# Kernel tuning notes

Measured on AMD Instinct MI355X. Metric: run time of the kernel, lower is better.

## Reference

```python
import jax, jax.numpy as jnp
import numpy as np

P = 3            # spline degree per axis (cubic)
NC = 64          # control points per axis
DOUT = 3         # output dimension of control points
NQ = 1_000_000   # number of query points


def open_uniform_knots(n, p):
    interior = np.linspace(0.0, 1.0, n - p + 1)
    return np.concatenate([np.zeros(p), interior, np.ones(p)]).astype(np.float32)  # len n+p+1


def bspline_basis(t, p, x):
    """Cox-de Boor basis. t:[n+p+1], x:[N] -> (i:[N,p+1] int, b:[N,p+1] float)."""
    n_basis = t.shape[0] - p - 1
    t_clamped = jnp.clip(x, t[p], t[-p - 1])
    k = jnp.searchsorted(t, t_clamped, side='right') - 1
    k = jnp.clip(k, p, n_basis - 1)                       # [N]
    i = k[:, None] + jnp.arange(-p, 1)                    # [N, p+1] global basis idx
    d = jnp.broadcast_to(jnp.eye(p + 1, dtype=x.dtype), (x.shape[0], p + 1, p + 1))
    for r in range(1, p + 1):
        j = jnp.arange(p, r - 1, -1)                      # [p-r+1]
        jk = j[None, :] + k[:, None]                      # [N, p-r+1]
        left = t[jk - p]
        right = t[jk + 1 - r]
        alpha = ((x[:, None] - left) / (right - left))[..., None]  # [N, p-r+1, 1]
        d = d.at[:, j].set((1.0 - alpha) * d[:, j - 1] + alpha * d[:, j])
    return i, d[:, p]                                     # basis values sum to 1


def setup_inputs() -> dict:
    key = jax.random.key(0)
    kq, kc = jax.random.split(key)
    queries = jax.random.uniform(kq, (NQ, 3), dtype=jnp.float32)
    control_points = jax.random.normal(kc, (NC * NC * NC, DOUT), dtype=jnp.float32)
    t = jnp.asarray(open_uniform_knots(NC, P))
    return {"queries": queries, "control_points": control_points,
            "tx": t, "ty": t, "tz": t}


def reference(queries, control_points, tx, ty, tz):
    px = py = pz = P
    ix, bx = bspline_basis(tx, px, queries[:, 0])   # [N,px+1]
    iy, by = bspline_basis(ty, py, queries[:, 1])
    iz, bz = bspline_basis(tz, pz, queries[:, 2])
    nx = tx.shape[0] - px - 1
    ny = ty.shape[0] - py - 1
    # flat index into [nx*ny*nz] control grid: ix + nx*(iy + ny*iz)
    flat_idx = (ix[:, :, None, None]
                + nx * (iy[:, None, :, None] + ny * iz[:, None, None, :]))  # [N,px+1,py+1,pz+1]
    cp_sel = control_points[flat_idx]                   # [N,px+1,py+1,pz+1,DOUT]
    y = jnp.einsum('na,nb,nc,nabcd->nd', bx, by, bz, cp_sel)
    return y
```

## Files before the change

kernel.cpp:

```cpp
#include <hip/hip_runtime.h>


#define NC 64
#define NSEG 61
#define NCELLS 512
#define WDIM 11
#define CAP 2560
#define CHUNK 512
#define NCHUNK 5
#define CHUNK_S 2048
#define OVF_CAP 4096
#define NB 512
#define FCHUNK 1024
#define FNCHUNK 3

typedef float vfloat4 __attribute__((ext_vector_type(4)));

__device__ __forceinline__ float rcpf(float x) {
#if __has_builtin(__builtin_amdgcn_rcpf)
  return __builtin_amdgcn_rcpf(x);
#else
  return 1.0f / x;
#endif
}

__device__ __forceinline__ int span_of(float x) {
  float xc = fminf(fmaxf(x, 0.0f), 1.0f);
  int j = (int)floorf(xc * (float)NSEG);
  return j > NSEG - 1 ? NSEG - 1 : (j < 0 ? 0 : j);
}

__device__ __forceinline__ float knotv(int i) {
  float v = (float)(i - 3) * (1.0f / (float)NSEG);
  return fminf(fmaxf(v, 0.0f), 1.0f);
}

__device__ __forceinline__ void basis4(float x, int j, float N[4]) {
  float xc = fminf(fmaxf(x, 0.0f), 1.0f);
  int k = j + 3;
  float left[4], right[4];
  N[0] = 1.0f;
#pragma unroll
  for (int jj = 1; jj <= 3; ++jj) {
    left[jj] = xc - knotv(k + 1 - jj);
    right[jj] = knotv(k + jj) - xc;
    float saved = 0.0f;
#pragma unroll
    for (int r = 0; r < jj; ++r) {
      float temp = N[r] * rcpf(right[r + 1] + left[jj - r]);
      N[r] = saved + right[r + 1] * temp;
      saved = left[jj - r] * temp;
    }
    N[jj] = saved;
  }
}

__device__ __forceinline__ void eval_point(float x, float y, float z, int jx,
                                           int jy, int jz,
                                           const float* __restrict__ cp,
                                           float o[3]) {
  float Nx[4], Ny[4], Nz[4];
  basis4(x, jx, Nx);
  basis4(y, jy, Ny);
  basis4(z, jz, Nz);
  float ax = 0, ay = 0, az = 0;
#pragma unroll 1
  for (int c = 0; c < 4; ++c) {
#pragma unroll
    for (int b = 0; b < 4; ++b) {
      float w = Ny[b] * Nz[c];
      const float* row = cp + 3 * (size_t)(jx + NC * (jy + b + NC * (jz + c)));
      vfloat4 f0, f1, f2;
      __builtin_memcpy(&f0, row + 0, 16);
      __builtin_memcpy(&f1, row + 4, 16);
      __builtin_memcpy(&f2, row + 8, 16);
      ax += w * (Nx[0] * f0.x + Nx[1] * f0.w + Nx[2] * f1.z + Nx[3] * f2.y);
      ay += w * (Nx[0] * f0.y + Nx[1] * f1.x + Nx[2] * f1.w + Nx[3] * f2.z);
      az += w * (Nx[0] * f0.z + Nx[1] * f1.y + Nx[2] * f2.x + Nx[3] * f2.w);
    }
  }
  o[0] = ax; o[1] = ay; o[2] = az;
}


__global__ __launch_bounds__(256) void scatter_capped(
    const float* __restrict__ q, int* __restrict__ gcursor,
    int* __restrict__ ovfcnt, float4* __restrict__ ovf,
    float4* __restrict__ sorted, int nq) {
  __shared__ int lh[NCELLS];
  __shared__ int lcur[NCELLS];
  int b = blockIdx.x, tid = threadIdx.x;
  for (int c = tid; c < NCELLS; c += 256) { lh[c] = 0; lcur[c] = 0; }
  __syncthreads();

  int s = b * CHUNK_S, e = min(nq, s + CHUNK_S);
  float xs[8], ys[8], zs[8];
  int cells[8];
#pragma unroll
  for (int it = 0; it < 8; ++it) {
    int i = s + it * 256 + tid;
    cells[it] = -1;
    if (i < e) {
      float xyz[3];
      __builtin_memcpy(xyz, q + 3 * (size_t)i, 12);
      xs[it] = xyz[0]; ys[it] = xyz[1]; zs[it] = xyz[2];
      int cell = (span_of(xyz[0]) >> 3) + 8 * (span_of(xyz[1]) >> 3) +
                 64 * (span_of(xyz[2]) >> 3);
      cells[it] = cell;
      atomicAdd(&lh[cell], 1);
    }
  }
  __syncthreads();
  for (int c = tid; c < NCELLS; c += 256) {
    int n = lh[c];
    lh[c] = n ? atomicAdd(&gcursor[c], n) : 0;
  }
  __syncthreads();
#pragma unroll
  for (int it = 0; it < 8; ++it) {
    int cell = cells[it];
    if (cell < 0) continue;
    int i = s + it * 256 + tid;
    int r = lh[cell] + atomicAdd(&lcur[cell], 1);
    if (r < CAP) {
      int jx = span_of(xs[it]), jy = span_of(ys[it]), jz = span_of(zs[it]);
      unsigned u = (unsigned)i | ((unsigned)(jx & 7) << 20) |
                   ((unsigned)(jy & 7) << 23) | ((unsigned)(jz & 7) << 26);
      sorted[(size_t)cell * CAP + r] =
          make_float4(xs[it], ys[it], zs[it], __int_as_float((int)u));
    } else {
      int p = atomicAdd(ovfcnt, 1);
      if (p < OVF_CAP)
        ovf[p] = make_float4(xs[it], ys[it], zs[it], __int_as_float(i));
    }
  }
}

__global__ __launch_bounds__(256) void eval_kernel(
    const float4* __restrict__ sorted, const int* __restrict__ cellbase,
    const int* __restrict__ cellcnt, const float* __restrict__ cp,
    float* __restrict__ out, int use_cap) {
  int cid = blockIdx.x / NCHUNK;
  int chunkid = blockIdx.x % NCHUNK;
  int cnt = cellcnt[cid];
  if (use_cap) cnt = min(cnt, CAP);
  if (chunkid * CHUNK >= cnt) return;
  size_t base = use_cap ? (size_t)cid * CAP : (size_t)cellbase[cid];
  int ox = (cid & 7) * 8, oy = ((cid >> 3) & 7) * 8, oz = (cid >> 6) * 8;

  __shared__ float4 lds[WDIM * WDIM * WDIM];
  for (int e = threadIdx.x; e < WDIM * WDIM * WDIM; e += 256) {
    int lx = e % WDIM, t = e / WDIM;
    int ly = t % WDIM, lz = t / WDIM;
    int gx = min(ox + lx, NC - 1), gy = min(oy + ly, NC - 1),
        gz = min(oz + lz, NC - 1);
    const float* p = cp + 3 * (size_t)(gx + NC * (gy + NC * gz));
    lds[e] = make_float4(p[0], p[1], p[2], 0.0f);
  }
  __syncthreads();

  for (int q0 = chunkid * CHUNK; q0 < cnt; q0 += NCHUNK * CHUNK) {
    int qend = min(cnt, q0 + CHUNK);
    for (int qi = q0 + (int)threadIdx.x; qi < qend; qi += 256) {
      float4 s = sorted[base + qi];
      unsigned u = (unsigned)__float_as_int(s.w);
      int oi = (int)(u & 0xFFFFFu);
      int lx0 = (int)((u >> 20) & 7), ly0 = (int)((u >> 23) & 7),
          lz0 = (int)((u >> 26) & 7);
      float Nx[4], Ny[4], Nz[4];
      basis4(s.x, ox + lx0, Nx);
      basis4(s.y, oy + ly0, Ny);
      basis4(s.z, oz + lz0, Nz);

      float ax = 0.0f, ay = 0.0f, az = 0.0f;
#pragma unroll
      for (int c = 0; c < 4; ++c) {
#pragma unroll
        for (int b = 0; b < 4; ++b) {
          float w = Ny[b] * Nz[c];
          const float4* row = &lds[((lz0 + c) * WDIM + (ly0 + b)) * WDIM + lx0];
          float4 p0 = row[0], p1 = row[1], p2 = row[2], p3 = row[3];
          ax += w * (Nx[0] * p0.x + Nx[1] * p1.x + Nx[2] * p2.x + Nx[3] * p3.x);
          ay += w * (Nx[0] * p0.y + Nx[1] * p1.y + Nx[2] * p2.y + Nx[3] * p3.y);
          az += w * (Nx[0] * p0.z + Nx[1] * p1.z + Nx[2] * p2.z + Nx[3] * p3.z);
        }
      }
      float o[3] = {ax, ay, az};
      __builtin_memcpy(out + 3 * (size_t)oi, o, 12);
    }
  }
}

__global__ __launch_bounds__(256) void ovf_kernel(const float4* __restrict__ ovf,
                                                  const int* __restrict__ ovfcnt,
                                                  const float* __restrict__ cp,
                                                  float* __restrict__ out) {
  int n = min(*ovfcnt, OVF_CAP);
  for (int i = blockIdx.x * 256 + threadIdx.x; i < n; i += gridDim.x * 256) {
    float4 s = ovf[i];
    int oi = __float_as_int(s.w);
    float o[3];
    eval_point(s.x, s.y, s.z, span_of(s.x), span_of(s.y), span_of(s.z), cp, o);
    __builtin_memcpy(out + 3 * (size_t)oi, o, 12);
  }
}


__global__ __launch_bounds__(256) void hist_kernel(const float* __restrict__ q,
                                                   int* __restrict__ histmat,
                                                   int nq, int chunk) {
  __shared__ int lh[NCELLS];
  for (int c = threadIdx.x; c < NCELLS; c += 256) lh[c] = 0;
  __syncthreads();
  int b = blockIdx.x;
  int s = b * chunk, e = min(nq, s + chunk);
  for (int i = s + (int)threadIdx.x; i < e; i += 256) {
    float xyz[3];
    __builtin_memcpy(xyz, q + 3 * (size_t)i, 12);
    int cell = (span_of(xyz[0]) >> 3) + 8 * (span_of(xyz[1]) >> 3) +
               64 * (span_of(xyz[2]) >> 3);
    atomicAdd(&lh[cell], 1);
  }
  __syncthreads();
  for (int c = threadIdx.x; c < NCELLS; c += 256)
    histmat[(size_t)c * NB + b] = lh[c];
}

__global__ __launch_bounds__(512) void rowscan_kernel(int* __restrict__ histmat,
                                                      int* __restrict__ cellsum) {
  __shared__ int sh[NB];
  int c = blockIdx.x, tid = threadIdx.x;
  int v = histmat[(size_t)c * NB + tid];
  sh[tid] = v;
  __syncthreads();
  for (int off = 1; off < NB; off <<= 1) {
    int t = (tid >= off) ? sh[tid - off] : 0;
    __syncthreads();
    sh[tid] += t;
    __syncthreads();
  }
  histmat[(size_t)c * NB + tid] = sh[tid] - v;
  if (tid == NB - 1) cellsum[c] = sh[tid];
}

__global__ __launch_bounds__(512) void cellscan_kernel(const int* __restrict__ cellsum,
                                                       int* __restrict__ cellbase) {
  __shared__ int sh[NCELLS];
  int tid = threadIdx.x;
  int v = cellsum[tid];
  sh[tid] = v;
  __syncthreads();
  for (int off = 1; off < NCELLS; off <<= 1) {
    int t = (tid >= off) ? sh[tid - off] : 0;
    __syncthreads();
    sh[tid] += t;
    __syncthreads();
  }
  cellbase[tid] = sh[tid] - v;
}

__global__ __launch_bounds__(256) void scatter_scan(const float* __restrict__ q,
                                                    const int* __restrict__ histmat,
                                                    const int* __restrict__ cellbase,
                                                    float4* __restrict__ sorted,
                                                    int nq, int chunk) {
  __shared__ int lcur[NCELLS];
  __shared__ int gbase[NCELLS];
  int b = blockIdx.x;
  for (int c = threadIdx.x; c < NCELLS; c += 256) {
    lcur[c] = 0;
    gbase[c] = cellbase[c] + histmat[(size_t)c * NB + b];
  }
  __syncthreads();
  int s = b * chunk, e = min(nq, s + chunk);
  for (int i = s + (int)threadIdx.x; i < e; i += 256) {
    float xyz[3];
    __builtin_memcpy(xyz, q + 3 * (size_t)i, 12);
    int jx = span_of(xyz[0]), jy = span_of(xyz[1]), jz = span_of(xyz[2]);
    int cell = (jx >> 3) + 8 * (jy >> 3) + 64 * (jz >> 3);
    int r = atomicAdd(&lcur[cell], 1);
    unsigned u = (unsigned)i | ((unsigned)(jx & 7) << 20) |
                 ((unsigned)(jy & 7) << 23) | ((unsigned)(jz & 7) << 26);
    sorted[gbase[cell] + r] =
        make_float4(xyz[0], xyz[1], xyz[2], __int_as_float((int)u));
  }
}

__global__ __launch_bounds__(256) void spline_direct_kernel(
    const float* __restrict__ q, const float* __restrict__ cp,
    float* __restrict__ out, int nq) {
  int i = blockIdx.x * 256 + threadIdx.x;
  if (i >= nq) return;
  float xyz[3];
  __builtin_memcpy(xyz, q + 3 * (size_t)i, 12);
  float o[3];
  eval_point(xyz[0], xyz[1], xyz[2], span_of(xyz[0]), span_of(xyz[1]),
             span_of(xyz[2]), cp, o);
  __builtin_memcpy(out + 3 * (size_t)i, o, 12);
}

extern "C" void kernel_launch(void* const* d_in, const int* in_sizes, int n_in,
                              void* d_out, int out_size, void* d_ws,
                              size_t ws_size, hipStream_t stream) {
  const float* queries = (const float*)d_in[0];
  const float* control = (const float*)d_in[1];
  float* out = (float*)d_out;
  int nq = in_sizes[0] / 3;

  size_t meta_c = (NCELLS + 1) * sizeof(int);
  size_t meta_cp = (meta_c + 15) & ~15ull;
  size_t need_c = meta_cp + (size_t)OVF_CAP * 16 + (size_t)NCELLS * CAP * 16;
  size_t meta_s = (size_t)NCELLS * NB * 4 + 2 * NCELLS * 4;
  size_t need_s = ((meta_s + 15) & ~15ull) + (size_t)nq * 16;

  if (nq < (1 << 20) && ws_size >= need_c) {
    int* gcursor = (int*)d_ws;
    int* ovfcnt = gcursor + NCELLS;
    float4* ovf = (float4*)((char*)d_ws + meta_cp);
    float4* sorted = ovf + OVF_CAP;
    hipMemsetAsync(d_ws, 0, meta_c, stream);
    int nb = (nq + CHUNK_S - 1) / CHUNK_S;
    scatter_capped<<<nb, 256, 0, stream>>>(queries, gcursor, ovfcnt, ovf,
                                           sorted, nq);
    eval_kernel<<<NCELLS * NCHUNK, 256, 0, stream>>>(sorted, gcursor, gcursor,
                                                     control, out, 1);
    ovf_kernel<<<4, 256, 0, stream>>>(ovf, ovfcnt, control, out);
  } else if (nq < (1 << 20) && ws_size >= need_s) {
    int* histmat = (int*)d_ws;
    int* cellsum = histmat + (size_t)NCELLS * NB;
    int* cellbase = cellsum + NCELLS;
    float4* sorted = (float4*)((char*)d_ws + ((meta_s + 15) & ~15ull));
    int chunk = (nq + NB - 1) / NB;
    hist_kernel<<<NB, 256, 0, stream>>>(queries, histmat, nq, chunk);
    rowscan_kernel<<<NCELLS, 512, 0, stream>>>(histmat, cellsum);
    cellscan_kernel<<<1, 512, 0, stream>>>(cellsum, cellbase);
    scatter_scan<<<NB, 256, 0, stream>>>(queries, histmat, cellbase, sorted,
                                         nq, chunk);
    eval_kernel<<<NCELLS * FNCHUNK, 256, 0, stream>>>(sorted, cellbase, cellsum,
                                                      control, out, 0);
  } else {
    spline_direct_kernel<<<(nq + 255) / 256, 256, 0, stream>>>(queries, control,
                                                               out, nq);
  }
}
```

Before: 141.8 us.

## Stage scatter writes in LDS by cell and sub-sort eval points by local span

The capped scatter kernel now does a block-local exclusive scan over cell counts and stages points in shared memory in cell order. It then writes them to the global bins in a second pass, so consecutive threads store to consecutive addresses instead of scattering randomly. The eval kernel bins the points of each chunk by their 9-bit local span key and processes them in that order, so a wavefront touches similar LDS control-point windows. The unused histogram/scan fallback path is removed. The added scans and syncs cost extra LDS traffic and barriers, and scatter_capped now uses about 44 KB of LDS, which may lower occupancy.

```diff
diff --git a/kernel.cpp b/kernel.cpp
--- a/kernel.cpp
+++ b/kernel.cpp
@@ -10,9 +10,6 @@
 #define NCHUNK 5
 #define CHUNK_S 2048
 #define OVF_CAP 4096
-#define NB 512
-#define FCHUNK 1024
-#define FNCHUNK 3
 
 typedef float vfloat4 __attribute__((ext_vector_type(4)));
 
@@ -82,20 +79,42 @@
   o[0] = ax; o[1] = ay; o[2] = az;
 }
 
+__device__ __forceinline__ void scan512_excl(int* arr) {
+  int tid = threadIdx.x;
+  int c0 = arr[tid], c1 = arr[tid + 256];
+#pragma unroll
+  for (int off = 1; off < 512; off <<= 1) {
+    int t0 = (tid >= off) ? arr[tid - off] : 0;
+    int t1 = ((tid + 256) >= off) ? arr[tid + 256 - off] : 0;
+    __syncthreads();
+    arr[tid] += t0;
+    arr[tid + 256] += t1;
+    __syncthreads();
+  }
+  arr[tid] -= c0;
+  arr[tid + 256] -= c1;
+  __syncthreads();
+}
+
 
 __global__ __launch_bounds__(256) void scatter_capped(
     const float* __restrict__ q, int* __restrict__ gcursor,
     int* __restrict__ ovfcnt, float4* __restrict__ ovf,
     float4* __restrict__ sorted, int nq) {
-  __shared__ int lh[NCELLS];
+  __shared__ int hist[NCELLS];
+  __shared__ int gb[NCELLS];
   __shared__ int lcur[NCELLS];
+  __shared__ float4 stage[CHUNK_S];
+  __shared__ int addr[CHUNK_S];
   int b = blockIdx.x, tid = threadIdx.x;
-  for (int c = tid; c < NCELLS; c += 256) { lh[c] = 0; lcur[c] = 0; }
+  for (int c = tid; c < NCELLS; c += 256) { hist[c] = 0; lcur[c] = 0; }
   __syncthreads();
 
   int s = b * CHUNK_S, e = min(nq, s + CHUNK_S);
+  int nblk = e - s;
   float xs[8], ys[8], zs[8];
   int cells[8];
+  unsigned us[8];
 #pragma unroll
   for (int it = 0; it < 8; ++it) {
     int i = s + it * 256 + tid;
@@ -104,90 +123,113 @@
       float xyz[3];
       __builtin_memcpy(xyz, q + 3 * (size_t)i, 12);
       xs[it] = xyz[0]; ys[it] = xyz[1]; zs[it] = xyz[2];
-      int cell = (span_of(xyz[0]) >> 3) + 8 * (span_of(xyz[1]) >> 3) +
-                 64 * (span_of(xyz[2]) >> 3);
-      cells[it] = cell;
-      atomicAdd(&lh[cell], 1);
-    }
-  }
-  __syncthreads();
-  for (int c = tid; c < NCELLS; c += 256) {
-    int n = lh[c];
-    lh[c] = n ? atomicAdd(&gcursor[c], n) : 0;
-  }
-  __syncthreads();
+      int jx = span_of(xyz[0]), jy = span_of(xyz[1]), jz = span_of(xyz[2]);
+      cells[it] = (jx >> 3) + 8 * (jy >> 3) + 64 * (jz >> 3);
+      us[it] = (unsigned)i | ((unsigned)(jx & 7) << 20) |
+               ((unsigned)(jy & 7) << 23) | ((unsigned)(jz & 7) << 26);
+      atomicAdd(&hist[cells[it]], 1);
+    }
+  }
+  __syncthreads();
+  int n0 = hist[tid], n1 = hist[tid + 256];
+  gb[tid] = n0 ? atomicAdd(&gcursor[tid], n0) : 0;
+  gb[tid + 256] = n1 ? atomicAdd(&gcursor[tid + 256], n1) : 0;
+  __syncthreads();
+  scan512_excl(hist);
 #pragma unroll
   for (int it = 0; it < 8; ++it) {
     int cell = cells[it];
     if (cell < 0) continue;
-    int i = s + it * 256 + tid;
-    int r = lh[cell] + atomicAdd(&lcur[cell], 1);
-    if (r < CAP) {
-      int jx = span_of(xs[it]), jy = span_of(ys[it]), jz = span_of(zs[it]);
-      unsigned u = (unsigned)i | ((unsigned)(jx & 7) << 20) |
-                   ((unsigned)(jy & 7) << 23) | ((unsigned)(jz & 7) << 26);
-      sorted[(size_t)cell * CAP + r] =
-          make_float4(xs[it], ys[it], zs[it], __int_as_float((int)u));
+    int rank = atomicAdd(&lcur[cell], 1);
+    int rloc = hist[cell] + rank;
+    int rg = gb[cell] + rank;
+    if (rg < CAP) {
+      stage[rloc] = make_float4(xs[it], ys[it], zs[it],
+                                __int_as_float((int)us[it]));
+      addr[rloc] = cell * CAP + rg;
     } else {
+      addr[rloc] = -1;
       int p = atomicAdd(ovfcnt, 1);
       if (p < OVF_CAP)
-        ovf[p] = make_float4(xs[it], ys[it], zs[it], __int_as_float(i));
-    }
-  }
-}
+        ovf[p] = make_float4(xs[it], ys[it], zs[it],
+                             __int_as_float((int)(us[it] & 0xFFFFFu)));
+    }
+  }
+  __syncthreads();
+  for (int j = tid; j < nblk; j += 256) {
+    int a = addr[j];
+    if (a >= 0) sorted[a] = stage[j];
+  }
+}
+
 
 __global__ __launch_bounds__(256) void eval_kernel(
-    const float4* __restrict__ sorted, const int* __restrict__ cellbase,
-    const int* __restrict__ cellcnt, const float* __restrict__ cp,
-    float* __restrict__ out, int use_cap) {
+    const float4* __restrict__ sorted, const int* __restrict__ cellcnt,
+    const float* __restrict__ cp, float* __restrict__ out) {
   int cid = blockIdx.x / NCHUNK;
   int chunkid = blockIdx.x % NCHUNK;
-  int cnt = cellcnt[cid];
-  if (use_cap) cnt = min(cnt, CAP);
-  if (chunkid * CHUNK >= cnt) return;
-  size_t base = use_cap ? (size_t)cid * CAP : (size_t)cellbase[cid];
+  int cnt = min(cellcnt[cid], CAP);
+  int q0 = chunkid * CHUNK;
+  if (q0 >= cnt) return;
+  int n = min(cnt - q0, CHUNK);
+  size_t base = (size_t)cid * CAP + q0;
   int ox = (cid & 7) * 8, oy = ((cid >> 3) & 7) * 8, oz = (cid >> 6) * 8;
+  int tid = threadIdx.x;
 
   __shared__ float4 lds[WDIM * WDIM * WDIM];
-  for (int e = threadIdx.x; e < WDIM * WDIM * WDIM; e += 256) {
-    int lx = e % WDIM, t = e / WDIM;
+  __shared__ int bins[CHUNK];
+  __shared__ unsigned short order[CHUNK];
+  for (int e2 = tid; e2 < WDIM * WDIM * WDIM; e2 += 256) {
+    int lx = e2 % WDIM, t = e2 / WDIM;
     int ly = t % WDIM, lz = t / WDIM;
     int gx = min(ox + lx, NC - 1), gy = min(oy + ly, NC - 1),
         gz = min(oz + lz, NC - 1);
     const float* p = cp + 3 * (size_t)(gx + NC * (gy + NC * gz));
-    lds[e] = make_float4(p[0], p[1], p[2], 0.0f);
-  }
-  __syncthreads();
-
-  for (int q0 = chunkid * CHUNK; q0 < cnt; q0 += NCHUNK * CHUNK) {
-    int qend = min(cnt, q0 + CHUNK);
-    for (int qi = q0 + (int)threadIdx.x; qi < qend; qi += 256) {
-      float4 s = sorted[base + qi];
-      unsigned u = (unsigned)__float_as_int(s.w);
-      int oi = (int)(u & 0xFFFFFu);
-      int lx0 = (int)((u >> 20) & 7), ly0 = (int)((u >> 23) & 7),
-          lz0 = (int)((u >> 26) & 7);
-      float Nx[4], Ny[4], Nz[4];
-      basis4(s.x, ox + lx0, Nx);
-      basis4(s.y, oy + ly0, Ny);
-      basis4(s.z, oz + lz0, Nz);
-
-      float ax = 0.0f, ay = 0.0f, az = 0.0f;
-#pragma unroll
-      for (int c = 0; c < 4; ++c) {
-#pragma unroll
-        for (int b = 0; b < 4; ++b) {
-          float w = Ny[b] * Nz[c];
-          const float4* row = &lds[((lz0 + c) * WDIM + (ly0 + b)) * WDIM + lx0];
-          float4 p0 = row[0], p1 = row[1], p2 = row[2], p3 = row[3];
-          ax += w * (Nx[0] * p0.x + Nx[1] * p1.x + Nx[2] * p2.x + Nx[3] * p3.x);
-          ay += w * (Nx[0] * p0.y + Nx[1] * p1.y + Nx[2] * p2.y + Nx[3] * p3.y);
-          az += w * (Nx[0] * p0.z + Nx[1] * p1.z + Nx[2] * p2.z + Nx[3] * p3.z);
-        }
+    lds[e2] = make_float4(p[0], p[1], p[2], 0.0f);
+  }
+  bins[tid] = 0;
+  bins[tid + 256] = 0;
+  int k0 = -1, k1 = -1, r0 = 0, r1 = 0;
+  if (tid < n)
+    k0 = (int)(((unsigned)__float_as_int(sorted[base + tid].w) >> 20) & 511u);
+  if (tid + 256 < n)
+    k1 = (int)(((unsigned)__float_as_int(sorted[base + tid + 256].w) >> 20) & 511u);
+  __syncthreads();
+  if (k0 >= 0) r0 = atomicAdd(&bins[k0], 1);
+  if (k1 >= 0) r1 = atomicAdd(&bins[k1], 1);
+  __syncthreads();
+  scan512_excl(bins);
+  if (k0 >= 0) order[bins[k0] + r0] = (unsigned short)tid;
+  if (k1 >= 0) order[bins[k1] + r1] = (unsigned short)(tid + 256);
+  __syncthreads();
+
+  for (int t2 = tid; t2 < n; t2 += 256) {
+    int lidx = order[t2];
+    float4 s = sorted[base + lidx];
+    unsigned u = (unsigned)__float_as_int(s.w);
+    int oi = (int)(u & 0xFFFFFu);
+    int lx0 = (int)((u >> 20) & 7), ly0 = (int)((u >> 23) & 7),
+        lz0 = (int)((u >> 26) & 7);
+    float Nx[4], Ny[4], Nz[4];
+    basis4(s.x, ox + lx0, Nx);
+    basis4(s.y, oy + ly0, Ny);
+    basis4(s.z, oz + lz0, Nz);
+
+    float ax = 0.0f, ay = 0.0f, az = 0.0f;
+#pragma unroll
+    for (int c = 0; c < 4; ++c) {
+#pragma unroll
+      for (int b = 0; b < 4; ++b) {
+        float w = Ny[b] * Nz[c];
+        const float4* row = &lds[((lz0 + c) * WDIM + (ly0 + b)) * WDIM + lx0];
+        float4 p0 = row[0], p1 = row[1], p2 = row[2], p3 = row[3];
+        ax += w * (Nx[0] * p0.x + Nx[1] * p1.x + Nx[2] * p2.x + Nx[3] * p3.x);
+        ay += w * (Nx[0] * p0.y + Nx[1] * p1.y + Nx[2] * p2.y + Nx[3] * p3.y);
+        az += w * (Nx[0] * p0.z + Nx[1] * p1.z + Nx[2] * p2.z + Nx[3] * p3.z);
       }
-      float o[3] = {ax, ay, az};
-      __builtin_memcpy(out + 3 * (size_t)oi, o, 12);
-    }
+    }
+    float o[3] = {ax, ay, az};
+    __builtin_memcpy(out + 3 * (size_t)oi, o, 12);
   }
 }
 
@@ -205,87 +247,6 @@
   }
 }
 
-
-__global__ __launch_bounds__(256) void hist_kernel(const float* __restrict__ q,
-                                                   int* __restrict__ histmat,
-                                                   int nq, int chunk) {
-  __shared__ int lh[NCELLS];
-  for (int c = threadIdx.x; c < NCELLS; c += 256) lh[c] = 0;
-  __syncthreads();
-  int b = blockIdx.x;
-  int s = b * chunk, e = min(nq, s + chunk);
-  for (int i = s + (int)threadIdx.x; i < e; i += 256) {
-    float xyz[3];
-    __builtin_memcpy(xyz, q + 3 * (size_t)i, 12);
-    int cell = (span_of(xyz[0]) >> 3) + 8 * (span_of(xyz[1]) >> 3) +
-               64 * (span_of(xyz[2]) >> 3);
-    atomicAdd(&lh[cell], 1);
-  }
-  __syncthreads();
-  for (int c = threadIdx.x; c < NCELLS; c += 256)
-    histmat[(size_t)c * NB + b] = lh[c];
-}
-
-__global__ __launch_bounds__(512) void rowscan_kernel(int* __restrict__ histmat,
-                                                      int* __restrict__ cellsum) {
-  __shared__ int sh[NB];
-  int c = blockIdx.x, tid = threadIdx.x;
-  int v = histmat[(size_t)c * NB + tid];
-  sh[tid] = v;
-  __syncthreads();
-  for (int off = 1; off < NB; off <<= 1) {
-    int t = (tid >= off) ? sh[tid - off] : 0;
-    __syncthreads();
-    sh[tid] += t;
-    __syncthreads();
-  }
-  histmat[(size_t)c * NB + tid] = sh[tid] - v;
-  if (tid == NB - 1) cellsum[c] = sh[tid];
-}
-
-__global__ __launch_bounds__(512) void cellscan_kernel(const int* __restrict__ cellsum,
-                                                       int* __restrict__ cellbase) {
-  __shared__ int sh[NCELLS];
-  int tid = threadIdx.x;
-  int v = cellsum[tid];
-  sh[tid] = v;
-  __syncthreads();
-  for (int off = 1; off < NCELLS; off <<= 1) {
-    int t = (tid >= off) ? sh[tid - off] : 0;
-    __syncthreads();
-    sh[tid] += t;
-    __syncthreads();
-  }
-  cellbase[tid] = sh[tid] - v;
-}
-
-__global__ __launch_bounds__(256) void scatter_scan(const float* __restrict__ q,
-                                                    const int* __restrict__ histmat,
-                                                    const int* __restrict__ cellbase,
-                                                    float4* __restrict__ sorted,
-                                                    int nq, int chunk) {
-  __shared__ int lcur[NCELLS];
-  __shared__ int gbase[NCELLS];
-  int b = blockIdx.x;
-  for (int c = threadIdx.x; c < NCELLS; c += 256) {
-    lcur[c] = 0;
-    gbase[c] = cellbase[c] + histmat[(size_t)c * NB + b];
-  }
-  __syncthreads();
-  int s = b * chunk, e = min(nq, s + chunk);
-  for (int i = s + (int)threadIdx.x; i < e; i += 256) {
-    float xyz[3];
-    __builtin_memcpy(xyz, q + 3 * (size_t)i, 12);
-    int jx = span_of(xyz[0]), jy = span_of(xyz[1]), jz = span_of(xyz[2]);
-    int cell = (jx >> 3) + 8 * (jy >> 3) + 64 * (jz >> 3);
-    int r = atomicAdd(&lcur[cell], 1);
-    unsigned u = (unsigned)i | ((unsigned)(jx & 7) << 20) |
-                 ((unsigned)(jy & 7) << 23) | ((unsigned)(jz & 7) << 26);
-    sorted[gbase[cell] + r] =
-        make_float4(xyz[0], xyz[1], xyz[2], __int_as_float((int)u));
-  }
-}
-
 __global__ __launch_bounds__(256) void spline_direct_kernel(
     const float* __restrict__ q, const float* __restrict__ cp,
     float* __restrict__ out, int nq) {
@@ -307,37 +268,22 @@
   float* out = (float*)d_out;
   int nq = in_sizes[0] / 3;
 
-  size_t meta_c = (NCELLS + 1) * sizeof(int);
-  size_t meta_cp = (meta_c + 15) & ~15ull;
-  size_t need_c = meta_cp + (size_t)OVF_CAP * 16 + (size_t)NCELLS * CAP * 16;
-  size_t meta_s = (size_t)NCELLS * NB * 4 + 2 * NCELLS * 4;
-  size_t need_s = ((meta_s + 15) & ~15ull) + (size_t)nq * 16;
-
-  if (nq < (1 << 20) && ws_size >= need_c) {
+  size_t meta = (NCELLS + 1) * sizeof(int);
+  size_t metap = (meta + 15) & ~15ull;
+  size_t need = metap + (size_t)OVF_CAP * 16 + (size_t)NCELLS * CAP * 16;
+
+  if (nq <= (1 << 20) && ws_size >= need) {
     int* gcursor = (int*)d_ws;
     int* ovfcnt = gcursor + NCELLS;
-    float4* ovf = (float4*)((char*)d_ws + meta_cp);
+    float4* ovf = (float4*)((char*)d_ws + metap);
     float4* sorted = ovf + OVF_CAP;
-    hipMemsetAsync(d_ws, 0, meta_c, stream);
+    hipMemsetAsync(d_ws, 0, meta, stream);
     int nb = (nq + CHUNK_S - 1) / CHUNK_S;
     scatter_capped<<<nb, 256, 0, stream>>>(queries, gcursor, ovfcnt, ovf,
                                            sorted, nq);
-    eval_kernel<<<NCELLS * NCHUNK, 256, 0, stream>>>(sorted, gcursor, gcursor,
-                                                     control, out, 1);
+    eval_kernel<<<NCELLS * NCHUNK, 256, 0, stream>>>(sorted, gcursor, control,
+                                                     out);
     ovf_kernel<<<4, 256, 0, stream>>>(ovf, ovfcnt, control, out);
-  } else if (nq < (1 << 20) && ws_size >= need_s) {
-    int* histmat = (int*)d_ws;
-    int* cellsum = histmat + (size_t)NCELLS * NB;
-    int* cellbase = cellsum + NCELLS;
-    float4* sorted = (float4*)((char*)d_ws + ((meta_s + 15) & ~15ull));
-    int chunk = (nq + NB - 1) / NB;
-    hist_kernel<<<NB, 256, 0, stream>>>(queries, histmat, nq, chunk);
-    rowscan_kernel<<<NCELLS, 512, 0, stream>>>(histmat, cellsum);
-    cellscan_kernel<<<1, 512, 0, stream>>>(cellsum, cellbase);
-    scatter_scan<<<NB, 256, 0, stream>>>(queries, histmat, cellbase, sorted,
-                                         nq, chunk);
-    eval_kernel<<<NCELLS * FNCHUNK, 256, 0, stream>>>(sorted, cellbase, cellsum,
-                                                      control, out, 0);
   } else {
     spline_direct_kernel<<<(nq + 255) / 256, 256, 0, stream>>>(queries, control,
                                                                out, nq);
```

Result: faster. 135.1 us (-4.7%).
